# Optimization experiments

Measured on AMD Instinct MI355X. Metric: run time of the kernel, lower is better.

Reference implementation:

```python
import jax, jax.numpy as jnp
import numpy as np

GRID, BOXN, LABELN = 14, 2, 20
COORD_RATE, NOOBJ_RATE = 5.0, 0.5
CELL = 1.0 / GRID  # cell_size = 1/grid_num
ALL_BOX = 5 * BOXN


def setup_inputs() -> dict:
    key = jax.random.key(0)
    k1, k2, k3 = jax.random.split(key, 3)
    B = 4096
    C = ALL_BOX + LABELN  # 30
    preds = jax.random.uniform(k1, (B, GRID, GRID, C), dtype=jnp.float32)
    truths = jax.random.uniform(k2, (B, GRID, GRID, C), dtype=jnp.float32)
    objm = jax.random.uniform(k3, (B, GRID, GRID)) < 0.08
    truths = truths.at[..., 4].set(jnp.where(objm, truths[..., 4], 0.0))
    return {"preds": preds, "truths": truths}


def _yolo_loss(preds, truths):
    B = preds.shape[0]
    dt = preds.dtype
    obj = truths[..., 4] > 0                                   # [B,S,S]
    pb = preds[..., :ALL_BOX].reshape(*preds.shape[:3], BOXN, 5)  # [B,S,S,Bx,5]
    tb = truths[..., 0:4]                                       # [B,S,S,4]

    # ---- IoU of every predicted box vs the truth box of its cell ----
    pc = CELL * pb[..., 0:2]; ph = pb[..., 2:4] / 2.0
    tc = CELL * tb[..., 0:2]; th = tb[..., 2:4] / 2.0
    p_lt, p_rb = pc - ph, pc + ph                               # [B,S,S,Bx,2]
    t_lt, t_rb = (tc - th)[..., None, :], (tc + th)[..., None, :]  # [B,S,S,1,2]
    lt = jnp.maximum(p_lt, t_lt)
    rb = jnp.minimum(p_rb, t_rb)
    wh = jnp.clip(rb - lt, 0.0, None)
    inter = wh[..., 0] * wh[..., 1]                             # [B,S,S,Bx]
    pa = (p_rb[..., 0] - p_lt[..., 0]) * (p_rb[..., 1] - p_lt[..., 1])
    ta = (t_rb[..., 0] - t_lt[..., 0]) * (t_rb[..., 1] - t_lt[..., 1])
    ious = inter / (pa + ta - inter)                            # [B,S,S,Bx]

    # ---- responsible-box selection (argmax IoU; ties broken by max conf) ----
    max_iou = jnp.max(ious, axis=-1)                            # [B,S,S]
    tied = ious == max_iou[..., None]
    n_tied = tied.sum(-1)
    conf = pb[..., 4]                                           # [B,S,S,Bx]
    ind_conf = jnp.argmax(jnp.where(tied, conf, -jnp.inf), axis=-1)
    ind_iou = jnp.argmax(ious, axis=-1)
    resp = jnp.where(n_tied > 1, ind_conf, ind_iou)             # [B,S,S]
    resp_oh = jax.nn.one_hot(resp, BOXN, dtype=bool)            # [B,S,S,Bx]

    w_obj = obj.astype(dt)
    pred_resp = jnp.take_along_axis(pb, resp[..., None, None], axis=3)[..., 0, :]  # [B,S,S,5]
    tbox5 = truths[..., 0:5]

    center_loss = jnp.sum(w_obj[..., None] * (pred_resp[..., 0:2] - tbox5[..., 0:2]) ** 2)
    size_loss = jnp.sum(w_obj[..., None] * (jnp.sqrt(pred_resp[..., 2:4]) - jnp.sqrt(tbox5[..., 2:4])) ** 2)
    t_conf = jax.lax.stop_gradient(max_iou)  # .item() in torch detaches the IoU target
    conf_resp_loss = jnp.sum(w_obj * (pred_resp[..., 4] - t_conf) ** 2)
    noresp = (obj[..., None] & (~resp_oh)).astype(dt)
    conf_noresp_loss = jnp.sum(noresp * conf ** 2)
    conf_noobj_loss = jnp.sum((~obj)[..., None].astype(dt) * conf ** 2)
    label_loss = jnp.sum(w_obj[..., None] * (preds[..., ALL_BOX:] - truths[..., ALL_BOX:]) ** 2)

    return (COORD_RATE * (center_loss + size_loss) + conf_resp_loss
            + NOOBJ_RATE * conf_noresp_loss + NOOBJ_RATE * conf_noobj_loss
            + label_loss) / B


def reference(preds, truths):
    return _yolo_loss(preds, truths)
```

## Files before the change

### kernel.cpp

```cpp
#include <hip/hip_runtime.h>
#include <math.h>

#define GRIDN   14
#define BOXN    2
#define LABELN  20
#define ALL_BOX 10
#define CCH     30

typedef float vfloat4 __attribute__((ext_vector_type(4)));

__global__ void yolo_zero_kernel(float* out, int n) {
    int i = blockIdx.x * blockDim.x + threadIdx.x;
    if (i < n) out[i] = 0.0f;
}

__device__ __forceinline__ float cell_loss(const float* p, const float* t) {
#pragma clang fp contract(off)
    const float CELL = (float)(1.0 / (double)GRIDN);

    const float tx = t[0], ty = t[1], tw = t[2], th_ = t[3], tconf = t[4];
    const bool obj = tconf > 0.0f;

    const float tcx = CELL * tx, tcy = CELL * ty;
    const float thx = tw * 0.5f, thy = th_ * 0.5f;
    const float tltx = tcx - thx, tlty = tcy - thy;
    const float trbx = tcx + thx, trby = tcy + thy;
    const float ta = (trbx - tltx) * (trby - tlty);

    float iou[BOXN], conf[BOXN];
#pragma unroll
    for (int b = 0; b < BOXN; ++b) {
        const float bx = p[b * 5 + 0], by = p[b * 5 + 1];
        const float bw = p[b * 5 + 2], bh = p[b * 5 + 3];
        conf[b] = p[b * 5 + 4];
        const float pcx = CELL * bx, pcy = CELL * by;
        const float phx = bw * 0.5f, phy = bh * 0.5f;
        const float pltx = pcx - phx, plty = pcy - phy;
        const float prbx = pcx + phx, prby = pcy + phy;
        const float ltx = fmaxf(pltx, tltx), lty = fmaxf(plty, tlty);
        const float rbx = fminf(prbx, trbx), rby = fminf(prby, trby);
        const float whx = fmaxf(rbx - ltx, 0.0f);
        const float why = fmaxf(rby - lty, 0.0f);
        const float inter = whx * why;
        const float pa = (prbx - pltx) * (prby - plty);
        iou[b] = inter / (pa + ta - inter);
    }

    const float max_iou = fmaxf(iou[0], iou[1]);
    bool r1;
    if (iou[0] == iou[1]) r1 = !(conf[0] >= conf[1]);
    else                  r1 = !(iou[0] > iou[1]);

    const float rx = r1 ? p[5] : p[0];
    const float ry = r1 ? p[6] : p[1];
    const float rw = r1 ? p[7] : p[2];
    const float rh = r1 ? p[8] : p[3];
    const float rc = r1 ? p[9] : p[4];

    const float dcx = rx - tx;
    const float dcy = ry - ty;
    const float center = dcx * dcx + dcy * dcy;

    const float dsx = sqrtf(rw) - sqrtf(tw);
    const float dsy = sqrtf(rh) - sqrtf(th_);
    const float size = dsx * dsx + dsy * dsy;

    const float dconf = rc - max_iou;
    const float conf_resp = dconf * dconf;

    const float c_other = r1 ? conf[0] : conf[1];
    const float conf_noresp = c_other * c_other;

    const float conf_noobj = conf[0] * conf[0] + conf[1] * conf[1];

    float label = 0.0f;
#pragma unroll
    for (int k = ALL_BOX; k < CCH; ++k) {
        const float d = p[k] - t[k];
        label += d * d;
    }

    const float w  = obj ? 1.0f : 0.0f;
    const float nw = obj ? 0.0f : 1.0f;
    return w * (5.0f * (center + size) + conf_resp + 0.5f * conf_noresp + label)
         + nw * (0.5f * conf_noobj);
}

__global__ __launch_bounds__(256, 2) void yolo_loss_kernel(
    const float* __restrict__ preds,
    const float* __restrict__ truths,
    float* __restrict__ out,
    int npairs)
{
#pragma clang fp contract(off)
    __shared__ float wsum[4];

    const int tid  = threadIdx.x;
    const int wave = tid >> 6;
    const int lane = tid & 63;

    const long long pair = (long long)blockIdx.x * blockDim.x + tid;

    float loss = 0.0f;
    if (pair < npairs) {
        const vfloat4* pp = (const vfloat4*)(preds  + pair * 60);
        const vfloat4* tp = (const vfloat4*)(truths + pair * 60);

        vfloat4 P4[15], T4[15];
#pragma unroll
        for (int i = 0; i < 15; ++i) P4[i] = __builtin_nontemporal_load(&pp[i]);
#pragma unroll
        for (int i = 0; i < 15; ++i) T4[i] = __builtin_nontemporal_load(&tp[i]);
        __builtin_amdgcn_sched_barrier(0);

        const float* P = (const float*)P4;
        const float* T = (const float*)T4;
        loss = cell_loss(P, T) + cell_loss(P + CCH, T + CCH);
    }

    float v = loss;
#pragma unroll
    for (int off = 32; off > 0; off >>= 1) v += __shfl_down(v, off, 64);
    if (lane == 0) wsum[wave] = v;
    __syncthreads();
    if (tid == 0) {
        const float s = (wsum[0] + wsum[1]) + (wsum[2] + wsum[3]);
        atomicAdd(out, s * (1.0f / 4096.0f));
    }
}

extern "C" void kernel_launch(void* const* d_in, const int* in_sizes, int n_in,
                              void* d_out, int out_size, void* d_ws, size_t ws_size,
                              hipStream_t stream) {
    const float* preds  = (const float*)d_in[0];
    const float* truths = (const float*)d_in[1];
    float* out = (float*)d_out;

    const int ncells = in_sizes[0] / CCH;
    const int npairs = ncells / 2;
    const int blocks = (npairs + 255) / 256;

    yolo_zero_kernel<<<(out_size + 255) / 256, 256, 0, stream>>>(out, out_size);
    yolo_loss_kernel<<<blocks, 256, 0, stream>>>(preds, truths, out, npairs);
}
```

Measured before the change: 254.6 us.

## Stage coalesced tiles through LDS in a persistent grid with register prefetch

Replaces per-thread strided 240-byte loads with fully coalesced float4 loads of a 256-cell tile of preds and truths. Each tile is staged into shared memory, and each thread computes one cell's loss from LDS. A fixed grid of 512 persistent blocks loops over tiles and prefetches the next tile into registers while the current one is computed. This reduces atomics and aims for better DRAM coalescing, at the cost of 60KB of LDS per block (lower occupancy), two barriers per tile, and LDS bank conflicts from the stride-30 reads. It assumes the cell count divides evenly by 256; any leftover cells would be dropped.

```diff
diff --git a/kernel.cpp b/kernel.cpp
--- a/kernel.cpp
+++ b/kernel.cpp
@@ -6,6 +6,11 @@
 #define LABELN  20
 #define ALL_BOX 10
 #define CCH     30
+
+#define TCELLS  256
+#define TF4     1920
+#define VTOT    3840
+#define PBLOCKS 512
 
 typedef float vfloat4 __attribute__((ext_vector_type(4)));
 
@@ -86,42 +91,61 @@
          + nw * (0.5f * conf_noobj);
 }
 
-__global__ __launch_bounds__(256, 2) void yolo_loss_kernel(
+__global__ __launch_bounds__(256) void yolo_loss_kernel(
     const float* __restrict__ preds,
     const float* __restrict__ truths,
     float* __restrict__ out,
-    int npairs)
+    int ntiles)
 {
 #pragma clang fp contract(off)
+    __shared__ vfloat4 sbuf[VTOT];
     __shared__ float wsum[4];
 
     const int tid  = threadIdx.x;
     const int wave = tid >> 6;
     const int lane = tid & 63;
 
-    const long long pair = (long long)blockIdx.x * blockDim.x + tid;
+    const vfloat4* pp = (const vfloat4*)preds;
+    const vfloat4* tp = (const vfloat4*)truths;
 
-    float loss = 0.0f;
-    if (pair < npairs) {
-        const vfloat4* pp = (const vfloat4*)(preds  + pair * 60);
-        const vfloat4* tp = (const vfloat4*)(truths + pair * 60);
+    vfloat4 R[15];
+    int tile = blockIdx.x;
 
-        vfloat4 P4[15], T4[15];
+    if (tile < ntiles) {
+        const long long g = (long long)tile * TF4;
 #pragma unroll
-        for (int i = 0; i < 15; ++i) P4[i] = __builtin_nontemporal_load(&pp[i]);
-#pragma unroll
-        for (int i = 0; i < 15; ++i) T4[i] = __builtin_nontemporal_load(&tp[i]);
-        __builtin_amdgcn_sched_barrier(0);
-
-        const float* P = (const float*)P4;
-        const float* T = (const float*)T4;
-        loss = cell_loss(P, T) + cell_loss(P + CCH, T + CCH);
+        for (int i = 0; i < 15; ++i) {
+            const int idx = i * 256 + tid;
+            R[i] = (idx < TF4) ? pp[g + idx] : tp[g + (idx - TF4)];
+        }
     }
 
-    float v = loss;
+    float acc = 0.0f;
+    for (; tile < ntiles; tile += PBLOCKS) {
+        const int next = tile + PBLOCKS;
+
+        __syncthreads();
 #pragma unroll
-    for (int off = 32; off > 0; off >>= 1) v += __shfl_down(v, off, 64);
-    if (lane == 0) wsum[wave] = v;
+        for (int i = 0; i < 15; ++i)
+            sbuf[i * 256 + tid] = R[i];
+
+        if (next < ntiles) {
+            const long long g = (long long)next * TF4;
+#pragma unroll
+            for (int i = 0; i < 15; ++i) {
+                const int idx = i * 256 + tid;
+                R[i] = (idx < TF4) ? pp[g + idx] : tp[g + (idx - TF4)];
+            }
+        }
+        __syncthreads();
+
+        const float* sf = (const float*)sbuf;
+        acc += cell_loss(sf + tid * CCH, sf + TF4 * 4 + tid * CCH);
+    }
+
+#pragma unroll
+    for (int off = 32; off > 0; off >>= 1) acc += __shfl_down(acc, off, 64);
+    if (lane == 0) wsum[wave] = acc;
     __syncthreads();
     if (tid == 0) {
         const float s = (wsum[0] + wsum[1]) + (wsum[2] + wsum[3]);
@@ -137,9 +161,8 @@
     float* out = (float*)d_out;
 
     const int ncells = in_sizes[0] / CCH;
-    const int npairs = ncells / 2;
-    const int blocks = (npairs + 255) / 256;
+    const int ntiles = ncells / TCELLS;
 
     yolo_zero_kernel<<<(out_size + 255) / 256, 256, 0, stream>>>(out, out_size);
-    yolo_loss_kernel<<<blocks, 256, 0, stream>>>(preds, truths, out, npairs);
+    yolo_loss_kernel<<<PBLOCKS, 256, 0, stream>>>(preds, truths, out, ntiles);
 }
```

New measurement: 204.5 us. 19.7% less time.
